# Kernel tuning notes

Hardware: AMD Instinct MI355X
Metric: run time of the kernel (lower is better)

## Reference

```python
import jax, jax.numpy as jnp
import numpy as np

B, T, HW, N, HID, K, OUT = 8, 64, 64, 64, 64, 2, 1
DT = 0.1


def setup_inputs() -> dict:
    key = jax.random.key(0)
    ks = jax.random.split(key, 16)
    nrm = lambda k, shape, s: jax.random.normal(k, shape, jnp.float32) * s
    return {
        "frames": jax.random.uniform(ks[0], (B, T, HW, HW, 3), jnp.float32),
        "adjacency": jax.random.uniform(ks[1], (B, T, N, N), jnp.float32) / N,
        "hidden0": jnp.zeros((B, N, HID), jnp.float32),
        "Wc1": nrm(ks[2], (32, 3, 3, 3), 0.3), "bc1": jnp.zeros(32, jnp.float32),
        "Wc2": nrm(ks[3], (64, 32, 3, 3), 0.08), "bc2": jnp.zeros(64, jnp.float32),
        "Wc3": nrm(ks[4], (128, 64, 3, 3), 0.06), "bc3": jnp.zeros(128, jnp.float32),
        "We": nrm(ks[5], (128, HID), 0.09), "be": jnp.zeros(HID, jnp.float32),
        "Wh": nrm(ks[6], (K + 1, HID, HID), 0.12),
        "Wx": nrm(ks[7], (K + 1, HID, HID), 0.12),
        "bg": jnp.zeros(HID, jnp.float32),
        "tau": jnp.ones(HID, jnp.float32),
        "Ap": nrm(ks[8], (HID,), 1.0),
        "Wd1": nrm(ks[9], (HID, 128), 0.12), "bd1": jnp.zeros(128, jnp.float32),
        "Wd2": nrm(ks[10], (128, 64), 0.09), "bd2": jnp.zeros(64, jnp.float32),
        "Wd3": nrm(ks[11], (64, OUT), 0.12), "bd3": jnp.zeros(OUT, jnp.float32),
    }


def _conv_relu(x, w, b, stride):
    # torch Conv2d(k=3, stride=2, padding=1) == explicit padding (1,1)
    y = jax.lax.conv_general_dilated(
        x, w, (stride, stride), [(1, 1), (1, 1)],
        dimension_numbers=("NCHW", "OIHW", "NCHW"))
    return jax.nn.relu(y + b[None, :, None, None])


def _forward(frames, adjacency, hidden0, Wc1, bc1, Wc2, bc2, Wc3, bc3,
             We, be, Wh, Wx, bg, tau, Ap, Wd1, bd1, Wd2, bd2, Wd3, bd3):
    Bn, Tn, Hh, Ww, C = frames.shape
    # faithful to torch .view(-1, C, H, W): raw memory reinterpretation
    x = frames.reshape(Bn * Tn, C, Hh, Ww)
    x = _conv_relu(x, Wc1, bc1, 2)   # [BT,32,32,32]
    x = _conv_relu(x, Wc2, bc2, 2)   # [BT,64,16,16]
    x = _conv_relu(x, Wc3, bc3, 2)   # [BT,128,8,8]; AdaptiveAvgPool2d((8,8)) is identity here
    feats = x.reshape(Bn, Tn, 128, 8, 8).transpose(0, 1, 3, 4, 2).reshape(Bn, Tn, 64, 128)
    node = feats @ We + be           # [B,T,N,HID]

    Kp = Wh.shape[0] - 1
    eye = jnp.eye(adjacency.shape[-1], dtype=frames.dtype)

    def step(h, inputs):
        xt, At = inputs              # [B,N,HID], [B,N,N]
        powers = [jnp.broadcast_to(eye, At.shape)]
        p = At
        for _ in range(Kp):          # static K-loop -> [I, A, ..., A^K]
            powers.append(p)
            p = jnp.matmul(p, At)
        S = jnp.stack(powers)        # [K+1,B,N,N]
        z = jnp.einsum("bnd,kde->kbne", h, Wh) + jnp.einsum("bnd,kde->kbne", xt, Wx)
        gc = jnp.einsum("kbnm,kbme->bne", S, z) + bg
        f = jnp.tanh(gc)
        h_next = h + DT * (-(1.0 / tau + f) * h + f * Ap)  # liquid time-constant Euler step
        m = h_next.mean(axis=1)      # [B,HID]
        d = jax.nn.relu(m @ Wd1 + bd1)
        d = jax.nn.relu(d @ Wd2 + bd2)
        c = d @ Wd3 + bd3            # [B,OUT]
        return h_next, c

    xs = (node.transpose(1, 0, 2, 3), adjacency.transpose(1, 0, 2, 3))
    final_h, controls = jax.lax.scan(step, hidden0, xs)
    controls = controls.transpose(1, 0, 2)  # [B,T,OUT]
    return controls, final_h


def reference(frames, adjacency, hidden0, Wc1, bc1, Wc2, bc2, Wc3, bc3,
              We, be, Wh, Wx, bg, tau, Ap, Wd1, bd1, Wd2, bd2, Wd3, bd3):
    return _forward(frames, adjacency, hidden0, Wc1, bc1, Wc2, bc2, Wc3, bc3,
                    We, be, Wh, Wx, bg, tau, Ap, Wd1, bd1, Wd2, bd2, Wd3, bd3)
```

## Files before the change

kernel.cpp:

```cpp
#include <hip/hip_runtime.h>
#include <hip/hip_bf16.h>

#define DT_C 0.1f
#define PS 72

typedef short bfrag __attribute__((ext_vector_type(8)));
typedef _Float16 hfrag __attribute__((ext_vector_type(8)));
typedef float f32x4 __attribute__((ext_vector_type(4)));

union FU { bfrag v; unsigned short s[8]; uint4 q; };
union HU { hfrag v; unsigned short s[8]; uint4 q; };

__device__ __forceinline__ unsigned short bf16_rn(float x) {
  union { float f; unsigned u; } v; v.f = x;
  unsigned r = v.u + 0x7fffu + ((v.u >> 16) & 1u);
  return (unsigned short)(r >> 16);
}
__device__ __forceinline__ float bf16_tof(unsigned short h) {
  union { unsigned u; float f; } v; v.u = ((unsigned)h) << 16; return v.f;
}
__device__ __forceinline__ unsigned short bfu(float x) {
  union { __hip_bfloat16 b; unsigned short u; } cv;
  cv.b = __float2bfloat16(x);
  return cv.u;
}
__device__ __forceinline__ float tanh_f(float x) {
  return 1.0f - 2.0f / (__expf(2.0f * x) + 1.0f);
}
__device__ __forceinline__ void h16split(float v, unsigned short& hu, unsigned short& lu) {
  union { _Float16 h; unsigned short u; } a, b;
  a.h = (_Float16)v;
  b.h = (_Float16)(v - (float)a.h);
  hu = a.u; lu = b.u;
}
__device__ __forceinline__ unsigned short h16hi(float v) {
  union { _Float16 h; unsigned short u; } a; a.h = (_Float16)v; return a.u;
}

__global__ __launch_bounds__(256) void wprep_k(const float* __restrict__ Wc2,
                                               const float* __restrict__ Wc3,
                                               const float* __restrict__ Wh,
                                               const float* __restrict__ We,
                                               const float* __restrict__ Wx,
                                               unsigned short* __restrict__ W2h,
                                               unsigned short* __restrict__ W2l,
                                               unsigned short* __restrict__ W3h,
                                               unsigned short* __restrict__ W3l,
                                               unsigned short* __restrict__ WTh,
                                               unsigned short* __restrict__ WTl,
                                               unsigned short* __restrict__ WeTh,
                                               unsigned short* __restrict__ WeTl,
                                               unsigned short* __restrict__ WxTh,
                                               unsigned short* __restrict__ WxTl) {
  int i = blockIdx.x * 256 + threadIdx.x;
  if (i < 18432) {
    int oc = i / 288, rem = i % 288, pos = rem >> 5, ic = rem & 31;
    float v = Wc2[oc*288 + ic*9 + pos];
    h16split(v, W2h[i], W2l[i]);
  } else if (i < 92160) {
    int j = i - 18432;
    int oc = j / 576, rem = j % 576, pos = rem >> 6, ic = rem & 63;
    float v = Wc3[oc*576 + ic*9 + pos];
    h16split(v, W3h[j], W3l[j]);
  } else if (i < 104448) {
    int j = i - 92160;
    int k3 = j >> 12, rem = j & 4095, din = rem >> 6, dout = rem & 63;
    float v = Wh[j];
    unsigned short hi = bf16_rn(v);
    WTh[k3*4096 + dout*64 + din] = hi;
    WTl[k3*4096 + dout*64 + din] = bf16_rn(v - bf16_tof(hi));
  } else if (i < 112640) {
    int j = i - 104448;
    int e = j >> 7, oc = j & 127;
    float v = We[oc*64 + e];
    h16split(v, WeTh[j], WeTl[j]);
  } else if (i < 124928) {
    int j = i - 112640;
    int k3 = j >> 12, rem = j & 4095, e = rem >> 6, din = rem & 63;
    float v = Wx[k3*4096 + din*64 + e];
    unsigned short hi = bf16_rn(v);
    WxTh[j] = hi;
    WxTl[j] = bf16_rn(v - bf16_tof(hi));
  }
}

__global__ __launch_bounds__(256) void conv1_k(const float* __restrict__ frames,
                                               const float* __restrict__ W,
                                               const float* __restrict__ bias,
                                               unsigned short* __restrict__ c1h) {
  __shared__ __align__(16) float sIn[12288];
  int bt = blockIdx.x, tid = threadIdx.x;
  const float4* src = (const float4*)(frames + (size_t)bt * 12288);
  for (int i = tid; i < 3072; i += 256) ((float4*)sIn)[i] = src[i];
  __syncthreads();
  for (int p = tid; p < 1024; p += 256) {
    int ho = p >> 5, wo = p & 31, hi0 = ho*2-1, wi0 = wo*2-1;
    int obase = (((ho*2 + (wo&1))*16 + (wo>>1)))*8;
    for (int ocb = 0; ocb < 4; ++ocb) {
      float acc[8];
      #pragma unroll
      for (int j = 0; j < 8; ++j) acc[j] = bias[ocb*8+j];
      for (int ic = 0; ic < 3; ++ic) {
        float win[9];
        #pragma unroll
        for (int kh = 0; kh < 3; ++kh) {
          int hi = hi0 + kh;
          #pragma unroll
          for (int kw = 0; kw < 3; ++kw) {
            int wi = wi0 + kw;
            win[kh*3+kw] = (hi>=0 && hi<64 && wi>=0 && wi<64) ? sIn[ic*4096 + hi*64 + wi] : 0.f;
          }
        }
        #pragma unroll
        for (int j = 0; j < 8; ++j) {
          const float* wp = W + (size_t)(ocb*8+j)*27 + ic*9;
          #pragma unroll
          for (int k = 0; k < 9; ++k) acc[j] += win[k] * wp[k];
        }
      }
      ushort hh[8];
      #pragma unroll
      for (int j = 0; j < 8; ++j) hh[j] = h16hi(fmaxf(acc[j], 0.f));
      *(uint4*)&c1h[(size_t)bt*32768 + ocb*8192 + obase] = *(uint4*)hh;
    }
  }
}

#define MFMAH(a, bb, cc) __builtin_amdgcn_mfma_f32_16x16x32_f16((a), (bb), (cc), 0, 0, 0)

__global__ __launch_bounds__(256) void conv2m_k(const unsigned short* __restrict__ c1h,
                                                const unsigned short* __restrict__ W2h,
                                                const unsigned short* __restrict__ W2l,
                                                const float* __restrict__ bias,
                                                unsigned short* __restrict__ c2h) {
  __shared__ __align__(16) unsigned short sH[32768];
  int bt = blockIdx.x, tid = threadIdx.x;
  {
    const uint4* gh = (const uint4*)(c1h + (size_t)bt*32768);
    for (int i = tid; i < 4096; i += 256) ((uint4*)sH)[i] = gh[i];
  }
  __syncthreads();
  int lane = tid & 63, w = tid >> 6, g = lane >> 4, c = lane & 15;
  f32x4 acc[4][4] = {};
  const uint4 z4 = make_uint4(0,0,0,0);
  #pragma unroll
  for (int pos = 0; pos < 9; ++pos) {
    const int kh = pos / 3, kw = pos % 3;
    HU Ah[4];
    #pragma unroll
    for (int m = 0; m < 4; ++m) {
      int pix = w*64 + m*16 + c;
      int ho = pix >> 4, wo = pix & 15;
      int hi = 2*ho - 1 + kh, wi = 2*wo - 1 + kw;
      bool ok = (hi >= 0) & (wi >= 0);
      int hic = ok ? hi : 0, wic = ok ? wi : 0;
      int a = (((g*32 + hic)*2 + (wic & 1))*16 + (wic >> 1))*8;
      uint4 vh = *(const uint4*)&sH[a];
      Ah[m].q = ok ? vh : z4;
    }
    HU Bh[4], Bl[4];
    #pragma unroll
    for (int n = 0; n < 4; ++n) {
      int off = (n*16 + c)*288 + pos*32 + g*8;
      Bh[n].q = *(const uint4*)(W2h + off);
      Bl[n].q = *(const uint4*)(W2l + off);
    }
    #pragma unroll
    for (int m = 0; m < 4; ++m)
      #pragma unroll
      for (int n = 0; n < 4; ++n) {
        acc[m][n] = MFMAH(Ah[m].v, Bh[n].v, acc[m][n]);
        acc[m][n] = MFMAH(Ah[m].v, Bl[n].v, acc[m][n]);
      }
  }
  #pragma unroll
  for (int n = 0; n < 4; ++n) {
    int oc = n*16 + c;
    float bv = bias[oc];
    int ks3 = oc >> 3, il = oc & 7;
    #pragma unroll
    for (int m = 0; m < 4; ++m) {
      #pragma unroll
      for (int r = 0; r < 4; ++r) {
        int pix = w*64 + m*16 + 4*g + r;
        int ho = pix >> 4, wo = pix & 15;
        float v = fmaxf(acc[m][n][r] + bv, 0.f);
        size_t dst = (size_t)bt*16384 + ((((ks3*16 + ho)*2 + (wo&1))*8 + (wo>>1)))*8 + il;
        c2h[dst] = h16hi(v);
      }
    }
  }
}

__global__ __launch_bounds__(256) void conv3e_k(const unsigned short* __restrict__ c2h,
                                                const unsigned short* __restrict__ W3h,
                                                const unsigned short* __restrict__ W3l,
                                                const float* __restrict__ bias,
                                                const unsigned short* __restrict__ WeTh,
                                                const unsigned short* __restrict__ WeTl,
                                                const float* __restrict__ be,
                                                float* __restrict__ node) {
  __shared__ __align__(16) unsigned short sH[16384];
  __shared__ __align__(16) unsigned short sF[64*136];
  int bt = blockIdx.x, tid = threadIdx.x;
  {
    const uint4* gh = (const uint4*)(c2h + (size_t)bt*16384);
    for (int i = tid; i < 2048; i += 256) ((uint4*)sH)[i] = gh[i];
  }
  __syncthreads();
  int lane = tid & 63, w = tid >> 6, g = lane >> 4, c = lane & 15;
  f32x4 acc[8] = {};
  const uint4 z4 = make_uint4(0,0,0,0);
  int pix = w*16 + c;
  int ho = pix >> 3, wo = pix & 7;
  #pragma unroll
  for (int pos = 0; pos < 9; ++pos) {
    const int kh = pos / 3, kw = pos % 3;
    int hi = 2*ho - 1 + kh, wi = 2*wo - 1 + kw;
    bool ok = (hi >= 0) & (wi >= 0);
    int hic = ok ? hi : 0, wic = ok ? wi : 0;
    #pragma unroll
    for (int ih = 0; ih < 2; ++ih) {
      int icg = ih*4 + g;
      int a = ((((icg*16 + hic)*2 + (wic & 1))*8 + (wic >> 1)))*8;
      HU Ah;
      uint4 vh = *(const uint4*)&sH[a];
      Ah.q = ok ? vh : z4;
      #pragma unroll
      for (int n = 0; n < 8; ++n) {
        int off = (n*16 + c)*576 + pos*64 + ih*32 + g*8;
        HU Bh, Bl;
        Bh.q = *(const uint4*)(W3h + off);
        Bl.q = *(const uint4*)(W3l + off);
        acc[n] = MFMAH(Ah.v, Bh.v, acc[n]);
        acc[n] = MFMAH(Ah.v, Bl.v, acc[n]);
      }
    }
  }
  #pragma unroll
  for (int n = 0; n < 8; ++n) {
    int oc = n*16 + c;
    float bv = bias[oc];
    #pragma unroll
    for (int r = 0; r < 4; ++r) {
      int po = w*16 + 4*g + r;
      sF[po*136 + oc] = h16hi(fmaxf(acc[n][r] + bv, 0.f));
    }
  }
  __syncthreads();
  f32x4 eacc[4] = {{0.f,0.f,0.f,0.f},{0.f,0.f,0.f,0.f},{0.f,0.f,0.f,0.f},{0.f,0.f,0.f,0.f}};
  #pragma unroll
  for (int kt = 0; kt < 4; ++kt) {
    HU Af;
    Af.q = *(const uint4*)&sF[(w*16 + c)*136 + kt*32 + g*8];
    #pragma unroll
    for (int n = 0; n < 4; ++n) {
      int off = (n*16 + c)*128 + kt*32 + g*8;
      HU Bh, Bl;
      Bh.q = *(const uint4*)(WeTh + off);
      Bl.q = *(const uint4*)(WeTl + off);
      eacc[n] = MFMAH(Af.v, Bh.v, eacc[n]);
      eacc[n] = MFMAH(Af.v, Bl.v, eacc[n]);
    }
  }
  #pragma unroll
  for (int n = 0; n < 4; ++n) {
    int e = n*16 + c;
    float bev = be[e];
    #pragma unroll
    for (int r = 0; r < 4; ++r) {
      int po = w*16 + 4*g + r;
      node[(size_t)bt*4096 + po*64 + e] = eacc[n][r] + bev;
    }
  }
}

#define MFMA(a, bb, cc) __builtin_amdgcn_mfma_f32_16x16x32_bf16((a), (bb), (cc), 0, 0, 0)

__global__ __launch_bounds__(512) void prepm_k(const float* __restrict__ adj,
                                               const float* __restrict__ node,
                                               const unsigned short* __restrict__ WxTh,
                                               const unsigned short* __restrict__ WxTl,
                                               unsigned short* __restrict__ Abf,
                                               unsigned short* __restrict__ A2bf,
                                               float* __restrict__ gxg) {
  __shared__ __align__(16) unsigned short sAh[64*PS], sAl[64*PS];
  __shared__ __align__(16) unsigned short sXh[64*PS], sXl[64*PS];
  __shared__ __align__(16) unsigned short sNh[64*PS], sNl[64*PS];
  __shared__ __align__(16) unsigned short sZh[64*PS], sZl[64*PS];
  int bt = blockIdx.x, tid = threadIdx.x;
  int lane = tid & 63, w = tid >> 6, g = lane >> 4, c = lane & 15;
  int mt = w & 3, nt0 = (w >> 2) * 2;
  int mrow = mt*16 + 4*g;
  for (int i = tid; i < 1024; i += 512) {
    int r = i >> 4, c0 = (i & 15) * 4;
    float4 av = ((const float4*)(adj + (size_t)bt*4096))[i];
    float4 nv = ((const float4*)(node + (size_t)bt*4096))[i];
    float aa[4] = {av.x, av.y, av.z, av.w};
    float nn[4] = {nv.x, nv.y, nv.z, nv.w};
    ushort4 ah4, al4, nh4, nl4;
    #pragma unroll
    for (int j = 0; j < 4; ++j) {
      unsigned short hi = bf16_rn(aa[j]);
      unsigned short lo = bf16_rn(aa[j] - bf16_tof(hi));
      ((unsigned short*)&ah4)[j] = hi;
      ((unsigned short*)&al4)[j] = lo;
      sXh[(c0+j)*PS + r] = hi;
      sXl[(c0+j)*PS + r] = lo;
      unsigned short nhi = bf16_rn(nn[j]);
      ((unsigned short*)&nh4)[j] = nhi;
      ((unsigned short*)&nl4)[j] = bf16_rn(nn[j] - bf16_tof(nhi));
    }
    *(ushort4*)&sAh[r*PS + c0] = ah4;
    *(ushort4*)&sAl[r*PS + c0] = al4;
    *(ushort4*)&sNh[r*PS + c0] = nh4;
    *(ushort4*)&sNl[r*PS + c0] = nl4;
    *(ushort4*)&Abf[(size_t)bt*4096 + r*64 + c0] = ah4;
  }
  __syncthreads();
  FU a_h[2], a_l[2], n_h[2], n_l[2];
  #pragma unroll
  for (int kt = 0; kt < 2; ++kt) {
    int ao = (mt*16 + c)*PS + kt*32 + 8*g;
    a_h[kt].q = *(const uint4*)&sAh[ao];
    a_l[kt].q = *(const uint4*)&sAl[ao];
    n_h[kt].q = *(const uint4*)&sNh[ao];
    n_l[kt].q = *(const uint4*)&sNl[ao];
  }
  f32x4 a2f[2] = {{0.f,0.f,0.f,0.f},{0.f,0.f,0.f,0.f}};
  f32x4 zf[2]  = {{0.f,0.f,0.f,0.f},{0.f,0.f,0.f,0.f}};
  #pragma unroll
  for (int tt = 0; tt < 2; ++tt) {
    int e = (nt0+tt)*16 + c;
    #pragma unroll
    for (int kt = 0; kt < 2; ++kt) {
      FU bh, bl;
      int bo = e*PS + kt*32 + 8*g;
      bh.q = *(const uint4*)&sXh[bo];
      bl.q = *(const uint4*)&sXl[bo];
      a2f[tt] = MFMA(a_h[kt].v, bh.v, a2f[tt]);
      a2f[tt] = MFMA(a_l[kt].v, bh.v, a2f[tt]);
      a2f[tt] = MFMA(a_h[kt].v, bl.v, a2f[tt]);
      FU wh, wl;
      int wo = 4096 + e*64 + kt*32 + 8*g;
      wh.q = *(const uint4*)(WxTh + wo);
      wl.q = *(const uint4*)(WxTl + wo);
      zf[tt] = MFMA(n_h[kt].v, wh.v, zf[tt]);
      zf[tt] = MFMA(n_l[kt].v, wh.v, zf[tt]);
      zf[tt] = MFMA(n_h[kt].v, wl.v, zf[tt]);
    }
  }
  __syncthreads();
  #pragma unroll
  for (int tt = 0; tt < 2; ++tt) {
    int e = (nt0+tt)*16 + c;
    ushort4 zh4, zl4;
    #pragma unroll
    for (int r = 0; r < 4; ++r) {
      float va = a2f[tt][r];
      unsigned short ahi = bf16_rn(va);
      sXh[(mrow+r)*PS + e] = ahi;
      sXl[(mrow+r)*PS + e] = bf16_rn(va - bf16_tof(ahi));
      A2bf[(size_t)bt*4096 + (mrow+r)*64 + e] = ahi;
      float vz = zf[tt][r];
      unsigned short zhi = bf16_rn(vz);
      ((unsigned short*)&zh4)[r] = zhi;
      ((unsigned short*)&zl4)[r] = bf16_rn(vz - bf16_tof(zhi));
    }
    *(ushort4*)&sZh[e*PS + mrow] = zh4;
    *(ushort4*)&sZl[e*PS + mrow] = zl4;
  }
  __syncthreads();
  f32x4 gacc[2] = {{0.f,0.f,0.f,0.f},{0.f,0.f,0.f,0.f}};
  #pragma unroll
  for (int tt = 0; tt < 2; ++tt) {
    int e = (nt0+tt)*16 + c;
    zf[tt][0] = 0.f; zf[tt][1] = 0.f; zf[tt][2] = 0.f; zf[tt][3] = 0.f;
    #pragma unroll
    for (int kt = 0; kt < 2; ++kt) {
      FU bh, bl;
      int bo = e*PS + kt*32 + 8*g;
      bh.q = *(const uint4*)&sZh[bo];
      bl.q = *(const uint4*)&sZl[bo];
      gacc[tt] = MFMA(a_h[kt].v, bh.v, gacc[tt]);
      gacc[tt] = MFMA(a_l[kt].v, bh.v, gacc[tt]);
      gacc[tt] = MFMA(a_h[kt].v, bl.v, gacc[tt]);
      FU wh, wl;
      int w0 = e*64 + kt*32 + 8*g;
      wh.q = *(const uint4*)(WxTh + w0);
      wl.q = *(const uint4*)(WxTl + w0);
      gacc[tt] = MFMA(n_h[kt].v, wh.v, gacc[tt]);
      gacc[tt] = MFMA(n_l[kt].v, wh.v, gacc[tt]);
      gacc[tt] = MFMA(n_h[kt].v, wl.v, gacc[tt]);
      int w2 = 8192 + e*64 + kt*32 + 8*g;
      wh.q = *(const uint4*)(WxTh + w2);
      wl.q = *(const uint4*)(WxTl + w2);
      zf[tt] = MFMA(n_h[kt].v, wh.v, zf[tt]);
      zf[tt] = MFMA(n_l[kt].v, wh.v, zf[tt]);
      zf[tt] = MFMA(n_h[kt].v, wl.v, zf[tt]);
    }
  }
  __syncthreads();
  #pragma unroll
  for (int tt = 0; tt < 2; ++tt) {
    int e = (nt0+tt)*16 + c;
    ushort4 zh4, zl4;
    #pragma unroll
    for (int r = 0; r < 4; ++r) {
      float vz = zf[tt][r];
      unsigned short zhi = bf16_rn(vz);
      ((unsigned short*)&zh4)[r] = zhi;
      ((unsigned short*)&zl4)[r] = bf16_rn(vz - bf16_tof(zhi));
    }
    *(ushort4*)&sZh[e*PS + mrow] = zh4;
    *(ushort4*)&sZl[e*PS + mrow] = zl4;
  }
  __syncthreads();
  FU p_h[2], p_l[2];
  #pragma unroll
  for (int kt = 0; kt < 2; ++kt) {
    int po = (mt*16 + c)*PS + kt*32 + 8*g;
    p_h[kt].q = *(const uint4*)&sXh[po];
    p_l[kt].q = *(const uint4*)&sXl[po];
  }
  #pragma unroll
  for (int tt = 0; tt < 2; ++tt) {
    int e = (nt0+tt)*16 + c;
    #pragma unroll
    for (int kt = 0; kt < 2; ++kt) {
      FU bh, bl;
      int bo = e*PS + kt*32 + 8*g;
      bh.q = *(const uint4*)&sZh[bo];
      bl.q = *(const uint4*)&sZl[bo];
      gacc[tt] = MFMA(p_h[kt].v, bh.v, gacc[tt]);
      gacc[tt] = MFMA(p_l[kt].v, bh.v, gacc[tt]);
      gacc[tt] = MFMA(p_h[kt].v, bl.v, gacc[tt]);
    }
    #pragma unroll
    for (int r = 0; r < 4; ++r)
      gxg[(size_t)bt*4096 + (mrow+r)*64 + e] = gacc[tt][r];
  }
}

__global__ __launch_bounds__(1024, 4) void seq2_k(
    const unsigned short* __restrict__ Abf, const unsigned short* __restrict__ A2bf,
    const float* __restrict__ gxg, const float* __restrict__ h0,
    const unsigned short* __restrict__ WTh, const unsigned short* __restrict__ WTl,
    const float* __restrict__ bg, const float* __restrict__ tau, const float* __restrict__ Apv,
    float* __restrict__ mout, float* __restrict__ out) {
  __shared__ unsigned short sHh[64*72];
  __shared__ unsigned short sA[2][64*72], sA2[2][64*72];
  __shared__ unsigned short sZ1[64*72], sZ2[64*72];
  __shared__ float sPart[64*17];
  int b = blockIdx.x, tid = threadIdx.x;
  int lane = tid & 63, w = tid >> 6, g = lane >> 4, c = lane & 15;
  int mt = w & 3, nt = w >> 2;
  int e = nt*16 + c;
  int mrow = mt*16 + 4*g;
  float itau = 1.f/tau[e], apv = Apv[e], bgv = bg[e];
  FU wf[3][2][2];
  #pragma unroll
  for (int k3 = 0; k3 < 3; ++k3)
    #pragma unroll
    for (int kt = 0; kt < 2; ++kt) {
      int off = k3*4096 + e*64 + kt*32 + 8*g;
      wf[k3][kt][0].q = *(const uint4*)(WTh + off);
      wf[k3][kt][1].q = *(const uint4*)(WTl + off);
    }
  float hm[4];
  #pragma unroll
  for (int r = 0; r < 4; ++r) hm[r] = h0[(size_t)b*4096 + (mrow+r)*64 + e];
  #pragma unroll
  for (int r = 0; r < 4; ++r) sHh[(mrow+r)*72 + e] = bfu(hm[r]);
  {
    int row = tid >> 4, k0 = (tid & 15) * 4;
    *(uint2*)&sA[0][row*72 + k0]  = *(const uint2*)(Abf  + (size_t)b*64*4096 + tid*4);
    *(uint2*)&sA2[0][row*72 + k0] = *(const uint2*)(A2bf + (size_t)b*64*4096 + tid*4);
  }
  __syncthreads();
  #pragma unroll 1
  for (int t = 0; t < 64; ++t) {
    int cur = t & 1;
    size_t bt = (size_t)b*64 + t;
    int tn = (t < 63) ? t + 1 : t;
    uint2 pa  = *(const uint2*)(Abf  + ((size_t)b*64 + tn)*4096 + tid*4);
    uint2 pa2 = *(const uint2*)(A2bf + ((size_t)b*64 + tn)*4096 + tid*4);
    float gxv[4];
    {
      const float* gp = gxg + bt*4096;
      #pragma unroll
      for (int r = 0; r < 4; ++r) gxv[r] = gp[(mrow+r)*64 + e];
    }
    FU ha[2];
    #pragma unroll
    for (int kt = 0; kt < 2; ++kt)
      ha[kt].q = *(const uint4*)&sHh[(mt*16 + c)*72 + kt*32 + 8*g];
    f32x4 a1 = {0.f,0.f,0.f,0.f}, a2 = {0.f,0.f,0.f,0.f};
    #pragma unroll
    for (int kt = 0; kt < 2; ++kt) {
      a1 = MFMA(ha[kt].v, wf[1][kt][0].v, a1);
      a1 = MFMA(ha[kt].v, wf[1][kt][1].v, a1);
      a2 = MFMA(ha[kt].v, wf[2][kt][0].v, a2);
      a2 = MFMA(ha[kt].v, wf[2][kt][1].v, a2);
    }
    {
      ushort4 o1, o2;
      o1.x = bfu(a1[0]); o1.y = bfu(a1[1]); o1.z = bfu(a1[2]); o1.w = bfu(a1[3]);
      o2.x = bfu(a2[0]); o2.y = bfu(a2[1]); o2.z = bfu(a2[2]); o2.w = bfu(a2[3]);
      *(ushort4*)&sZ1[e*72 + mrow] = o1;
      *(ushort4*)&sZ2[e*72 + mrow] = o2;
    }
    __syncthreads();
    f32x4 acc = {0.f,0.f,0.f,0.f};
    #pragma unroll
    for (int kt = 0; kt < 2; ++kt) {
      FU aA, aA2, z1f, z2f;
      int ao = (mt*16 + c)*72 + kt*32 + 8*g;
      aA.q  = *(const uint4*)&sA[cur][ao];
      aA2.q = *(const uint4*)&sA2[cur][ao];
      z1f.q = *(const uint4*)&sZ1[e*72 + kt*32 + 8*g];
      z2f.q = *(const uint4*)&sZ2[e*72 + kt*32 + 8*g];
      acc = MFMA(ha[kt].v, wf[0][kt][0].v, acc);
      acc = MFMA(ha[kt].v, wf[0][kt][1].v, acc);
      acc = MFMA(aA.v,  z1f.v, acc);
      acc = MFMA(aA2.v, z2f.v, acc);
    }
    float ps = 0.f;
    #pragma unroll
    for (int r = 0; r < 4; ++r) {
      float gc = acc[r] + gxv[r] + bgv;
      float f = tanh_f(gc);
      float hn = hm[r] + DT_C * (-(itau + f) * hm[r] + f * apv);
      hm[r] = hn;
      ps += hn;
      sHh[(mrow+r)*72 + e] = bfu(hn);
    }
    sPart[e*17 + mt*4 + g] = ps;
    {
      int row = tid >> 4, k0 = (tid & 15) * 4;
      *(uint2*)&sA[cur^1][row*72 + k0]  = pa;
      *(uint2*)&sA2[cur^1][row*72 + k0] = pa2;
    }
    __syncthreads();
    if (lane < 4) {
      int ee = w*4 + lane;
      float s = 0.f;
      #pragma unroll
      for (int j = 0; j < 16; ++j) s += sPart[ee*17 + j];
      mout[bt*64 + ee] = s * (1.0f / 64.0f);
    }
  }
  #pragma unroll
  for (int r = 0; r < 4; ++r)
    out[512 + (size_t)b*4096 + (mrow+r)*64 + e] = hm[r];
}

__global__ __launch_bounds__(128) void dec_k(const float* __restrict__ mout,
                                             const float* __restrict__ Wd1, const float* __restrict__ bd1,
                                             const float* __restrict__ Wd2, const float* __restrict__ bd2,
                                             const float* __restrict__ Wd3, const float* __restrict__ bd3,
                                             float* __restrict__ out) {
  __shared__ float sm[64], sd1[128], sd2[64];
  int bt = blockIdx.x, tid = threadIdx.x;
  if (tid < 64) sm[tid] = mout[(size_t)bt*64 + tid];
  __syncthreads();
  {
    float a = bd1[tid];
    #pragma unroll 8
    for (int e = 0; e < 64; ++e) a += sm[e] * Wd1[e*128 + tid];
    sd1[tid] = fmaxf(a, 0.f);
  }
  __syncthreads();
  if (tid < 64) {
    float a = bd2[tid];
    #pragma unroll 8
    for (int i = 0; i < 128; ++i) a += sd1[i] * Wd2[i*64 + tid];
    sd2[tid] = fmaxf(a, 0.f);
  }
  __syncthreads();
  if (tid < 64) {
    float p = sd2[tid] * Wd3[tid];
    #pragma unroll
    for (int off = 32; off > 0; off >>= 1) p += __shfl_down(p, off, 64);
    if (tid == 0) out[bt] = p + bd3[0];
  }
}

extern "C" void kernel_launch(void* const* d_in, const int* in_sizes, int n_in,
                              void* d_out, int out_size, void* d_ws, size_t ws_size,
                              hipStream_t stream) {
  const float* frames = (const float*)d_in[0];
  const float* adj    = (const float*)d_in[1];
  const float* h0     = (const float*)d_in[2];
  const float* Wc1 = (const float*)d_in[3];  const float* bc1 = (const float*)d_in[4];
  const float* Wc2 = (const float*)d_in[5];  const float* bc2 = (const float*)d_in[6];
  const float* Wc3 = (const float*)d_in[7];  const float* bc3 = (const float*)d_in[8];
  const float* We  = (const float*)d_in[9];  const float* be  = (const float*)d_in[10];
  const float* Wh  = (const float*)d_in[11]; const float* Wx  = (const float*)d_in[12];
  const float* bg  = (const float*)d_in[13]; const float* tau = (const float*)d_in[14];
  const float* Ap  = (const float*)d_in[15];
  const float* Wd1 = (const float*)d_in[16]; const float* bd1 = (const float*)d_in[17];
  const float* Wd2 = (const float*)d_in[18]; const float* bd2 = (const float*)d_in[19];
  const float* Wd3 = (const float*)d_in[20]; const float* bd3 = (const float*)d_in[21];

  float* ws = (float*)d_ws;
  unsigned short* c1h = (unsigned short*)(ws);
  unsigned short* c2h = (unsigned short*)(ws + 16777216);
  unsigned short* W2h = (unsigned short*)(ws + 20971520);
  unsigned short* W2l = (unsigned short*)(ws + 20980736);
  unsigned short* W3h = (unsigned short*)(ws + 20989952);
  unsigned short* W3l = (unsigned short*)(ws + 21026816);
  unsigned short* WTh = (unsigned short*)(ws + 21063680);
  unsigned short* WTl = (unsigned short*)(ws + 21069824);
  unsigned short* WeTh = (unsigned short*)(ws + 21075968);
  unsigned short* WeTl = (unsigned short*)(ws + 21080064);
  unsigned short* WxTh = (unsigned short*)(ws + 21084160);
  unsigned short* WxTl = (unsigned short*)(ws + 21090304);
  float* node = ws + 4194304;
  float* gx   = ws + 6291456;
  unsigned short* Abf  = (unsigned short*)(ws + 8388608);
  unsigned short* A2bf = (unsigned short*)(ws + 9437184);
  float* mo   = ws + 10485760;
  float* out  = (float*)d_out;

  wprep_k <<<488, 256, 0, stream>>>(Wc2, Wc3, Wh, We, Wx, W2h, W2l, W3h, W3l,
                                    WTh, WTl, WeTh, WeTl, WxTh, WxTl);
  conv1_k <<<512, 256, 0, stream>>>(frames, Wc1, bc1, c1h);
  conv2m_k<<<512, 256, 0, stream>>>(c1h, W2h, W2l, bc2, c2h);
  conv3e_k<<<512, 256, 0, stream>>>(c2h, W3h, W3l, bc3, WeTh, WeTl, be, node);
  prepm_k <<<512, 512, 0, stream>>>(adj, node, WxTh, WxTl, Abf, A2bf, gx);
  seq2_k  <<<8,  1024, 0, stream>>>(Abf, A2bf, gx, h0, WTh, WTl, bg, tau, Ap, mo, out);
  dec_k   <<<512, 128, 0, stream>>>(mo, Wd1, bd1, Wd2, bd2, Wd3, bd3, out);
}
```

Measured before the change: 293.4 us.

## Rewrite conv1 as an fp16 MFMA implicit GEMM with split-weight precision

```diff
diff --git a/kernel.cpp b/kernel.cpp
--- a/kernel.cpp
+++ b/kernel.cpp
@@ -42,6 +42,7 @@
                                                const float* __restrict__ Wh,
                                                const float* __restrict__ We,
                                                const float* __restrict__ Wx,
+                                               const float* __restrict__ Wc1,
                                                unsigned short* __restrict__ W2h,
                                                unsigned short* __restrict__ W2l,
                                                unsigned short* __restrict__ W3h,
@@ -51,7 +52,9 @@
                                                unsigned short* __restrict__ WeTh,
                                                unsigned short* __restrict__ WeTl,
                                                unsigned short* __restrict__ WxTh,
-                                               unsigned short* __restrict__ WxTl) {
+                                               unsigned short* __restrict__ WxTl,
+                                               unsigned short* __restrict__ W1h,
+                                               unsigned short* __restrict__ W1l) {
   int i = blockIdx.x * 256 + threadIdx.x;
   if (i < 18432) {
     int oc = i / 288, rem = i % 288, pos = rem >> 5, ic = rem & 31;
@@ -81,52 +84,81 @@
     unsigned short hi = bf16_rn(v);
     WxTh[j] = hi;
     WxTl[j] = bf16_rn(v - bf16_tof(hi));
-  }
-}
-
-__global__ __launch_bounds__(256) void conv1_k(const float* __restrict__ frames,
-                                               const float* __restrict__ W,
-                                               const float* __restrict__ bias,
-                                               unsigned short* __restrict__ c1h) {
-  __shared__ __align__(16) float sIn[12288];
+  } else if (i < 125952) {
+    int j = i - 124928;
+    int oc = j >> 5, k = j & 31;
+    float v = 0.f;
+    if (k < 27) { int pos = k / 3, ic = k % 3; v = Wc1[oc*27 + ic*9 + pos]; }
+    h16split(v, W1h[j], W1l[j]);
+  }
+}
+
+#define MFMAH(a, bb, cc) __builtin_amdgcn_mfma_f32_16x16x32_f16((a), (bb), (cc), 0, 0, 0)
+
+__global__ __launch_bounds__(512) void conv1m_k(const float* __restrict__ frames,
+                                                const unsigned short* __restrict__ W1h,
+                                                const unsigned short* __restrict__ W1l,
+                                                const float* __restrict__ bias,
+                                                unsigned short* __restrict__ c1h) {
+  __shared__ __align__(16) unsigned short sIn[12288];
   int bt = blockIdx.x, tid = threadIdx.x;
-  const float4* src = (const float4*)(frames + (size_t)bt * 12288);
-  for (int i = tid; i < 3072; i += 256) ((float4*)sIn)[i] = src[i];
-  __syncthreads();
-  for (int p = tid; p < 1024; p += 256) {
-    int ho = p >> 5, wo = p & 31, hi0 = ho*2-1, wi0 = wo*2-1;
-    int obase = (((ho*2 + (wo&1))*16 + (wo>>1)))*8;
-    for (int ocb = 0; ocb < 4; ++ocb) {
-      float acc[8];
+  {
+    const float4* src = (const float4*)(frames + (size_t)bt * 12288);
+    for (int i = tid; i < 3072; i += 512) {
+      float4 v = src[i];
+      ushort4 h;
+      h.x = h16hi(v.x); h.y = h16hi(v.y); h.z = h16hi(v.z); h.w = h16hi(v.w);
+      *(ushort4*)&sIn[i*4] = h;
+    }
+  }
+  __syncthreads();
+  int lane = tid & 63, w = tid >> 6, g = lane >> 4, c = lane & 15;
+  HU Bh[2], Bl[2];
+  #pragma unroll
+  for (int n = 0; n < 2; ++n) {
+    Bh[n].q = *(const uint4*)(W1h + (n*16 + c)*32 + g*8);
+    Bl[n].q = *(const uint4*)(W1l + (n*16 + c)*32 + g*8);
+  }
+  float bv[2] = {bias[c], bias[16 + c]};
+  #pragma unroll 1
+  for (int im = 0; im < 8; ++im) {
+    int mi = w*8 + im;
+    int p = mi*16 + c;
+    int ho = p >> 5, wo = p & 31;
+    HU Af;
+    #pragma unroll
+    for (int j = 0; j < 8; ++j) {
+      int k = 8*g + j;
+      unsigned short v = 0;
+      if (k < 27) {
+        int pos = k / 3, ic = k % 3;
+        int hi = 2*ho - 1 + pos/3, wi = 2*wo - 1 + pos%3;
+        v = (hi >= 0 && wi >= 0) ? sIn[ic*4096 + hi*64 + wi] : (unsigned short)0;
+      }
+      Af.s[j] = v;
+    }
+    f32x4 acc[2] = {{0.f,0.f,0.f,0.f},{0.f,0.f,0.f,0.f}};
+    #pragma unroll
+    for (int n = 0; n < 2; ++n) {
+      acc[n] = MFMAH(Af.v, Bh[n].v, acc[n]);
+      acc[n] = MFMAH(Af.v, Bl[n].v, acc[n]);
+    }
+    #pragma unroll
+    for (int n = 0; n < 2; ++n) {
+      int oc = n*16 + c;
+      int ks3 = oc >> 3, il = oc & 7;
       #pragma unroll
-      for (int j = 0; j < 8; ++j) acc[j] = bias[ocb*8+j];
-      for (int ic = 0; ic < 3; ++ic) {
-        float win[9];
-        #pragma unroll
-        for (int kh = 0; kh < 3; ++kh) {
-          int hi = hi0 + kh;
-          #pragma unroll
-          for (int kw = 0; kw < 3; ++kw) {
-            int wi = wi0 + kw;
-            win[kh*3+kw] = (hi>=0 && hi<64 && wi>=0 && wi<64) ? sIn[ic*4096 + hi*64 + wi] : 0.f;
-          }
-        }
-        #pragma unroll
-        for (int j = 0; j < 8; ++j) {
-          const float* wp = W + (size_t)(ocb*8+j)*27 + ic*9;
-          #pragma unroll
-          for (int k = 0; k < 9; ++k) acc[j] += win[k] * wp[k];
-        }
+      for (int r = 0; r < 4; ++r) {
+        int po = mi*16 + 4*g + r;
+        int ho2 = po >> 5, wo2 = po & 31;
+        float v = fmaxf(acc[n][r] + bv[n], 0.f);
+        size_t dst = (size_t)bt*32768 + ks3*8192
+                   + ((size_t)((ho2*2 + (wo2&1))*16 + (wo2>>1)))*8 + il;
+        c1h[dst] = h16hi(v);
       }
-      ushort hh[8];
-      #pragma unroll
-      for (int j = 0; j < 8; ++j) hh[j] = h16hi(fmaxf(acc[j], 0.f));
-      *(uint4*)&c1h[(size_t)bt*32768 + ocb*8192 + obase] = *(uint4*)hh;
-    }
-  }
-}
-
-#define MFMAH(a, bb, cc) __builtin_amdgcn_mfma_f32_16x16x32_f16((a), (bb), (cc), 0, 0, 0)
+    }
+  }
+}
 
 __global__ __launch_bounds__(256) void conv2m_k(const unsigned short* __restrict__ c1h,
                                                 const unsigned short* __restrict__ W2h,
@@ -616,6 +648,8 @@
   unsigned short* WeTl = (unsigned short*)(ws + 21080064);
   unsigned short* WxTh = (unsigned short*)(ws + 21084160);
   unsigned short* WxTl = (unsigned short*)(ws + 21090304);
+  unsigned short* W1h  = (unsigned short*)(ws + 21096448);
+  unsigned short* W1l  = (unsigned short*)(ws + 21096960);
   float* node = ws + 4194304;
   float* gx   = ws + 6291456;
   unsigned short* Abf  = (unsigned short*)(ws + 8388608);
@@ -623,9 +657,9 @@
   float* mo   = ws + 10485760;
   float* out  = (float*)d_out;
 
-  wprep_k <<<488, 256, 0, stream>>>(Wc2, Wc3, Wh, We, Wx, W2h, W2l, W3h, W3l,
-                                    WTh, WTl, WeTh, WeTl, WxTh, WxTl);
-  conv1_k <<<512, 256, 0, stream>>>(frames, Wc1, bc1, c1h);
+  wprep_k <<<492, 256, 0, stream>>>(Wc2, Wc3, Wh, We, Wx, Wc1, W2h, W2l, W3h, W3l,
+                                    WTh, WTl, WeTh, WeTl, WxTh, WxTl, W1h, W1l);
+  conv1m_k<<<512, 512, 0, stream>>>(frames, W1h, W1l, bc1, c1h);
   conv2m_k<<<512, 256, 0, stream>>>(c1h, W2h, W2l, bc2, c2h);
   conv3e_k<<<512, 256, 0, stream>>>(c2h, W3h, W3l, bc3, WeTh, WeTl, be, node);
   prepm_k <<<512, 512, 0, stream>>>(adj, node, WxTh, WxTl, Abf, A2bf, gx);
```

Measured after the change: 264.3 us. -9.9%, faster.
